# Kernel optimization log

Hardware: AMD Instinct MI355X
Metric: run time of the kernel (lower is better)

## Reference

```python
import jax, jax.numpy as jnp
import numpy as np

BATCH, IN_F, OUT_F = 4096, 1024, 1024


def setup_inputs() -> dict:
    key = jax.random.key(0)
    kx, kw = jax.random.split(key)
    x = jax.random.normal(kx, (BATCH, IN_F, 4), dtype=jnp.float32)
    weight = jax.random.normal(kw, (OUT_F, IN_F, 4), dtype=jnp.float32) * 0.01
    bias = jnp.zeros((OUT_F, 4), dtype=jnp.float32)
    return {"x": x, "weight": weight, "bias": bias}


def reference(x, weight, bias):
    # x: (batch, in, 4) quaternions; weight: (out, in, 4); bias: (out, 4)
    # Hamilton product broadcast over (batch, out, in) then summed over in ==
    # 16 signed real GEMMs contracting the `in` dimension.
    ar, ai, aj, ak = x[..., 0], x[..., 1], x[..., 2], x[..., 3]          # (b, i)
    br, bi, bj, bk = weight[..., 0], weight[..., 1], weight[..., 2], weight[..., 3]  # (o, i)

    mm = lambda a, w: jnp.einsum('bi,oi->bo', a, w)

    out_r = mm(ar, br) - mm(ai, bi) - mm(aj, bj) - mm(ak, bk)
    out_i = mm(ar, bi) + mm(ai, br) + mm(aj, bk) - mm(ak, bj)
    out_j = mm(ar, bj) - mm(ai, bk) + mm(aj, br) + mm(ak, bi)
    out_k = mm(ar, bk) + mm(ai, bj) - mm(aj, bi) + mm(ak, br)

    out = jnp.stack([out_r, out_i, out_j, out_k], axis=-1)  # (b, o, 4)
    return out + bias
```

## Files before the change

### kernel.cpp

```cpp
#include <hip/hip_runtime.h>


typedef __bf16 bf16x8 __attribute__((ext_vector_type(8)));
typedef __bf16 bf16x4 __attribute__((ext_vector_type(4)));
typedef float floatx4 __attribute__((ext_vector_type(4)));

constexpr int M = 4096;
constexpr int N = 4096;
constexpr int K = 4096;
constexpr int BM = 128, BN = 128, BK = 32;

__global__ void cvt_x_kernel(const float* __restrict__ x, __bf16* __restrict__ o) {
    const size_t i = (size_t)blockIdx.x * blockDim.x + threadIdx.x;
    const float4* xp = (const float4*)x;
    float4 a = xp[2 * i];
    float4 b = xp[2 * i + 1];
    bf16x8 v;
    v[0] = (__bf16)a.x; v[1] = (__bf16)a.y; v[2] = (__bf16)a.z; v[3] = (__bf16)a.w;
    v[4] = (__bf16)b.x; v[5] = (__bf16)b.y; v[6] = (__bf16)b.z; v[7] = (__bf16)b.w;
    *(bf16x8*)(o + 8 * i) = v;
}

__global__ void expand_w_kernel(const float* __restrict__ w, __bf16* __restrict__ wb) {
    const int idx = blockIdx.x * blockDim.x + threadIdx.x;
    const int o = idx >> 10;
    const int i = idx & 1023;
    float4 q = ((const float4*)w)[idx];
    bf16x4 r0, r1, r2, r3;
    r0[0] = (__bf16)q.x;  r0[1] = (__bf16)(-q.y); r0[2] = (__bf16)(-q.z); r0[3] = (__bf16)(-q.w);
    r1[0] = (__bf16)q.y;  r1[1] = (__bf16)q.x;   r1[2] = (__bf16)q.w;    r1[3] = (__bf16)(-q.z);
    r2[0] = (__bf16)q.z;  r2[1] = (__bf16)(-q.w); r2[2] = (__bf16)q.x;   r2[3] = (__bf16)q.y;
    r3[0] = (__bf16)q.w;  r3[1] = (__bf16)q.z;   r3[2] = (__bf16)(-q.y); r3[3] = (__bf16)q.x;
    __bf16* base = wb + (size_t)(o * 4) * K + i * 4;
    *(bf16x4*)(base)                 = r0;
    *(bf16x4*)(base + (size_t)K)     = r1;
    *(bf16x4*)(base + (size_t)2 * K) = r2;
    *(bf16x4*)(base + (size_t)3 * K) = r3;
}

__device__ __forceinline__ void gload_lds16(const __bf16* g, __bf16* l) {
    __builtin_amdgcn_global_load_lds(
        (const __attribute__((address_space(1))) void*)g,
        (__attribute__((address_space(3))) void*)l, 16, 0, 0);
}

__global__ void qgemm_kernel(const __bf16* __restrict__ A,
                             const __bf16* __restrict__ B,
                             const float* __restrict__ bias,
                             float* __restrict__ C) {
    __shared__ __bf16 As[BM][BK];
    __shared__ __bf16 Bs[BN][BK];

    const int tid  = threadIdx.x;
    const int wave = tid >> 6;
    const int lane = tid & 63;
    const int bm = blockIdx.y * BM;
    const int bn = blockIdx.x * BN;
    const int wm = (wave & 1) * 64;
    const int wn = (wave >> 1) * 64;

    const int ldrow = lane >> 2;
    const int ldcol = (lane & 3) * 8;

    const __bf16* ag0 = A + (size_t)(bm + wave * 16 + ldrow) * K + ldcol;
    const __bf16* ag1 = ag0 + (size_t)64 * K;
    const __bf16* bg0 = B + (size_t)(bn + wave * 16 + ldrow) * K + ldcol;
    const __bf16* bg1 = bg0 + (size_t)64 * K;

    __bf16* as0 = &As[wave * 16][0];
    __bf16* as1 = &As[64 + wave * 16][0];
    __bf16* bs0 = &Bs[wave * 16][0];
    __bf16* bs1 = &Bs[64 + wave * 16][0];

    floatx4 acc[4][4] = {};

    const int fl = lane & 15;
    const int fk = (lane >> 4) * 8;

    for (int k0 = 0; k0 < K; k0 += BK) {
        gload_lds16(ag0 + k0, as0);
        gload_lds16(ag1 + k0, as1);
        gload_lds16(bg0 + k0, bs0);
        gload_lds16(bg1 + k0, bs1);
        __syncthreads();

        bf16x8 af[4], bfr[4];
#pragma unroll
        for (int t = 0; t < 4; ++t)
            af[t] = *(const bf16x8*)&As[wm + t * 16 + fl][fk];
#pragma unroll
        for (int t = 0; t < 4; ++t)
            bfr[t] = *(const bf16x8*)&Bs[wn + t * 16 + fl][fk];

#pragma unroll
        for (int mt = 0; mt < 4; ++mt)
#pragma unroll
            for (int nt = 0; nt < 4; ++nt)
                acc[mt][nt] = __builtin_amdgcn_mfma_f32_16x16x32_bf16(
                    af[mt], bfr[nt], acc[mt][nt], 0, 0, 0);
        __syncthreads();
    }

#pragma unroll
    for (int mt = 0; mt < 4; ++mt) {
        const int row = bm + wm + mt * 16 + (lane >> 4) * 4;
#pragma unroll
        for (int nt = 0; nt < 4; ++nt) {
            const int col = bn + wn + nt * 16 + fl;
            const float bv = bias[col];
            float* cp = C + (size_t)row * N + col;
#pragma unroll
            for (int r = 0; r < 4; ++r)
                cp[(size_t)r * N] = acc[mt][nt][r] + bv;
        }
    }
}

extern "C" void kernel_launch(void* const* d_in, const int* in_sizes, int n_in,
                              void* d_out, int out_size, void* d_ws, size_t ws_size,
                              hipStream_t stream) {
    const float* x    = (const float*)d_in[0];
    const float* w    = (const float*)d_in[1];
    const float* bias = (const float*)d_in[2];
    float* out = (float*)d_out;

    __bf16* Abf  = (__bf16*)d_ws;
    __bf16* Wbig = (__bf16*)((char*)d_ws + (size_t)M * K * 2);

    cvt_x_kernel<<<(M * K / 8) / 256, 256, 0, stream>>>(x, Abf);
    expand_w_kernel<<<(1024 * 1024) / 256, 256, 0, stream>>>(w, Wbig);

    dim3 grid(N / BN, M / BM);
    qgemm_kernel<<<grid, 256, 0, stream>>>(Abf, Wbig, bias, out);
}
```

Before: 289.6 us.

## Switch GEMM to 32x32x16 MFMA and merge prep kernels into one launch

The GEMM inner loop now uses 32x32x16 bf16 MFMA tiles (2x2 per wave over two K sub-steps) instead of 16x16x32 tiles (4x4 per wave). This needs fewer LDS fragment reads per MFMA and fewer instructions. The epilogue is remapped to the 32x32 accumulator layout. Separately, the x conversion and weight expansion kernels are fused into one launch, and the weight path now handles two quaternions per thread with 16-byte stores. The larger MFMA shape may cause more LDS bank conflicts, and the epilogue stores are more strided.

Result: slower. 297.3 us (+2.7%).

```diff
diff --git a/kernel.cpp b/kernel.cpp
--- a/kernel.cpp
+++ b/kernel.cpp
@@ -2,40 +2,49 @@
 
 
 typedef __bf16 bf16x8 __attribute__((ext_vector_type(8)));
-typedef __bf16 bf16x4 __attribute__((ext_vector_type(4)));
-typedef float floatx4 __attribute__((ext_vector_type(4)));
+typedef float floatx16 __attribute__((ext_vector_type(16)));
 
 constexpr int M = 4096;
 constexpr int N = 4096;
 constexpr int K = 4096;
 constexpr int BM = 128, BN = 128, BK = 32;
 
-__global__ void cvt_x_kernel(const float* __restrict__ x, __bf16* __restrict__ o) {
-    const size_t i = (size_t)blockIdx.x * blockDim.x + threadIdx.x;
-    const float4* xp = (const float4*)x;
-    float4 a = xp[2 * i];
-    float4 b = xp[2 * i + 1];
-    bf16x8 v;
-    v[0] = (__bf16)a.x; v[1] = (__bf16)a.y; v[2] = (__bf16)a.z; v[3] = (__bf16)a.w;
-    v[4] = (__bf16)b.x; v[5] = (__bf16)b.y; v[6] = (__bf16)b.z; v[7] = (__bf16)b.w;
-    *(bf16x8*)(o + 8 * i) = v;
-}
+constexpr int CVT_BLOCKS = (M * K / 8) / 256;
+constexpr int EXP_BLOCKS = (1024 * 1024 / 2) / 256;
 
-__global__ void expand_w_kernel(const float* __restrict__ w, __bf16* __restrict__ wb) {
-    const int idx = blockIdx.x * blockDim.x + threadIdx.x;
-    const int o = idx >> 10;
-    const int i = idx & 1023;
-    float4 q = ((const float4*)w)[idx];
-    bf16x4 r0, r1, r2, r3;
-    r0[0] = (__bf16)q.x;  r0[1] = (__bf16)(-q.y); r0[2] = (__bf16)(-q.z); r0[3] = (__bf16)(-q.w);
-    r1[0] = (__bf16)q.y;  r1[1] = (__bf16)q.x;   r1[2] = (__bf16)q.w;    r1[3] = (__bf16)(-q.z);
-    r2[0] = (__bf16)q.z;  r2[1] = (__bf16)(-q.w); r2[2] = (__bf16)q.x;   r2[3] = (__bf16)q.y;
-    r3[0] = (__bf16)q.w;  r3[1] = (__bf16)q.z;   r3[2] = (__bf16)(-q.y); r3[3] = (__bf16)q.x;
-    __bf16* base = wb + (size_t)(o * 4) * K + i * 4;
-    *(bf16x4*)(base)                 = r0;
-    *(bf16x4*)(base + (size_t)K)     = r1;
-    *(bf16x4*)(base + (size_t)2 * K) = r2;
-    *(bf16x4*)(base + (size_t)3 * K) = r3;
+__global__ void prep_kernel(const float* __restrict__ x, const float* __restrict__ w,
+                            __bf16* __restrict__ A, __bf16* __restrict__ Wb) {
+    const int b = blockIdx.x;
+    if (b < CVT_BLOCKS) {
+        const size_t i = (size_t)b * 256 + threadIdx.x;
+        const float4* xp = (const float4*)x;
+        float4 a = xp[2 * i];
+        float4 c = xp[2 * i + 1];
+        bf16x8 v;
+        v[0] = (__bf16)a.x; v[1] = (__bf16)a.y; v[2] = (__bf16)a.z; v[3] = (__bf16)a.w;
+        v[4] = (__bf16)c.x; v[5] = (__bf16)c.y; v[6] = (__bf16)c.z; v[7] = (__bf16)c.w;
+        *(bf16x8*)(A + 8 * i) = v;
+    } else {
+        const int idx = (b - CVT_BLOCKS) * 256 + threadIdx.x;
+        const int o  = idx >> 9;
+        const int ip = (idx & 511) * 2;
+        float4 q0 = ((const float4*)w)[o * 1024 + ip];
+        float4 q1 = ((const float4*)w)[o * 1024 + ip + 1];
+        __bf16* base = Wb + (size_t)(o * 4) * K + ip * 4;
+        bf16x8 r;
+        r[0] = (__bf16)q0.x; r[1] = (__bf16)(-q0.y); r[2] = (__bf16)(-q0.z); r[3] = (__bf16)(-q0.w);
+        r[4] = (__bf16)q1.x; r[5] = (__bf16)(-q1.y); r[6] = (__bf16)(-q1.z); r[7] = (__bf16)(-q1.w);
+        *(bf16x8*)(base) = r;
+        r[0] = (__bf16)q0.y; r[1] = (__bf16)q0.x; r[2] = (__bf16)q0.w; r[3] = (__bf16)(-q0.z);
+        r[4] = (__bf16)q1.y; r[5] = (__bf16)q1.x; r[6] = (__bf16)q1.w; r[7] = (__bf16)(-q1.z);
+        *(bf16x8*)(base + (size_t)K) = r;
+        r[0] = (__bf16)q0.z; r[1] = (__bf16)(-q0.w); r[2] = (__bf16)q0.x; r[3] = (__bf16)q0.y;
+        r[4] = (__bf16)q1.z; r[5] = (__bf16)(-q1.w); r[6] = (__bf16)q1.x; r[7] = (__bf16)q1.y;
+        *(bf16x8*)(base + (size_t)2 * K) = r;
+        r[0] = (__bf16)q0.w; r[1] = (__bf16)q0.z; r[2] = (__bf16)(-q0.y); r[3] = (__bf16)q0.x;
+        r[4] = (__bf16)q1.w; r[5] = (__bf16)q1.z; r[6] = (__bf16)(-q1.y); r[7] = (__bf16)q1.x;
+        *(bf16x8*)(base + (size_t)3 * K) = r;
+    }
 }
 
 __device__ __forceinline__ void gload_lds16(const __bf16* g, __bf16* l) {
@@ -72,10 +81,10 @@
     __bf16* bs0 = &Bs[wave * 16][0];
     __bf16* bs1 = &Bs[64 + wave * 16][0];
 
-    floatx4 acc[4][4] = {};
+    floatx16 acc[2][2] = {};
 
-    const int fl = lane & 15;
-    const int fk = (lane >> 4) * 8;
+    const int fl = lane & 31;
+    const int fk = (lane >> 5) * 8;
 
     for (int k0 = 0; k0 < K; k0 += BK) {
         gload_lds16(ag0 + k0, as0);
@@ -84,34 +93,39 @@
         gload_lds16(bg1 + k0, bs1);
         __syncthreads();
 
-        bf16x8 af[4], bfr[4];
 #pragma unroll
-        for (int t = 0; t < 4; ++t)
-            af[t] = *(const bf16x8*)&As[wm + t * 16 + fl][fk];
+        for (int ks = 0; ks < 2; ++ks) {
+            const int kk = ks * 16 + fk;
+            bf16x8 af[2], bfr[2];
 #pragma unroll
-        for (int t = 0; t < 4; ++t)
-            bfr[t] = *(const bf16x8*)&Bs[wn + t * 16 + fl][fk];
-
+            for (int t = 0; t < 2; ++t)
+                af[t] = *(const bf16x8*)&As[wm + t * 32 + fl][kk];
 #pragma unroll
-        for (int mt = 0; mt < 4; ++mt)
+            for (int t = 0; t < 2; ++t)
+                bfr[t] = *(const bf16x8*)&Bs[wn + t * 32 + fl][kk];
 #pragma unroll
-            for (int nt = 0; nt < 4; ++nt)
-                acc[mt][nt] = __builtin_amdgcn_mfma_f32_16x16x32_bf16(
-                    af[mt], bfr[nt], acc[mt][nt], 0, 0, 0);
+            for (int mt = 0; mt < 2; ++mt)
+#pragma unroll
+                for (int nt = 0; nt < 2; ++nt)
+                    acc[mt][nt] = __builtin_amdgcn_mfma_f32_32x32x16_bf16(
+                        af[mt], bfr[nt], acc[mt][nt], 0, 0, 0);
+        }
         __syncthreads();
     }
 
 #pragma unroll
-    for (int mt = 0; mt < 4; ++mt) {
-        const int row = bm + wm + mt * 16 + (lane >> 4) * 4;
+    for (int mt = 0; mt < 2; ++mt) {
+        const int row_base = bm + wm + mt * 32 + 4 * (lane >> 5);
 #pragma unroll
-        for (int nt = 0; nt < 4; ++nt) {
-            const int col = bn + wn + nt * 16 + fl;
+        for (int nt = 0; nt < 2; ++nt) {
+            const int col = bn + wn + nt * 32 + fl;
             const float bv = bias[col];
-            float* cp = C + (size_t)row * N + col;
+            float* cp = C + (size_t)row_base * N + col;
 #pragma unroll
-            for (int r = 0; r < 4; ++r)
-                cp[(size_t)r * N] = acc[mt][nt][r] + bv;
+            for (int reg = 0; reg < 16; ++reg) {
+                const int roff = (reg & 3) + 8 * (reg >> 2);
+                cp[(size_t)roff * N] = acc[mt][nt][reg] + bv;
+            }
         }
     }
 }
@@ -127,8 +141,7 @@
     __bf16* Abf  = (__bf16*)d_ws;
     __bf16* Wbig = (__bf16*)((char*)d_ws + (size_t)M * K * 2);
 
-    cvt_x_kernel<<<(M * K / 8) / 256, 256, 0, stream>>>(x, Abf);
-    expand_w_kernel<<<(1024 * 1024) / 256, 256, 0, stream>>>(w, Wbig);
+    prep_kernel<<<CVT_BLOCKS + EXP_BLOCKS, 256, 0, stream>>>(x, w, Abf, Wbig);
 
     dim3 grid(N / BN, M / BM);
     qgemm_kernel<<<grid, 256, 0, stream>>>(Abf, Wbig, bias, out);
```
